# Kernel optimization log

Hardware: AMD Instinct MI355X
Metric: run time of the kernel (lower is better)

The kernel has to match this reference:

```python
import jax, jax.numpy as jnp
import numpy as np

NUM_NODES_G1 = 60000
NUM_NODES_G2 = 50000
NUM_REL = 16
NUM_BASES = 4
DIM = 128  # node_dim == hidden_dim == final_dim
L_COMMON = 100


def _concept_layer(x, edge_index):
    # Gather-based concept propagation: x_i <- x_i + mean_{j in N(i)} x_j
    src, dst = edge_index[0], edge_index[1]
    n = x.shape[0]
    agg = jax.ops.segment_sum(x[src], dst, num_segments=n)
    deg = jax.ops.segment_sum(jnp.ones((src.shape[0],), x.dtype), dst, num_segments=n)
    return x + agg / jnp.clip(deg, 1.0)[:, None]


def _rgcn_layer(x, edge_index, edge_type, basis, comp, root, bias):
    # Basis-decomposed RGCN: out_i = x_i @ root + bias + sum_r (1/|N_i^r|) sum_{j in N_i^r} x_j @ W_r,
    # W_r = sum_b comp[r,b] * basis[b]. Reorder: scatter comp-weighted x[src] per basis, then one GEMM per basis.
    src, dst = edge_index[0], edge_index[1]
    n = x.shape[0]
    e = src.shape[0]
    seg = dst * NUM_REL + edge_type  # per-(node, relation) bucket
    cnt = jax.ops.segment_sum(jnp.ones((e,), x.dtype), seg, num_segments=n * NUM_REL)
    norm = 1.0 / jnp.clip(cnt, 1.0)
    coef = comp[edge_type] * norm[seg][:, None]  # [E, B]
    xsrc = x[src]  # [E, D] -- dominant gather traffic
    out = x @ root + bias
    for b in range(NUM_BASES):  # small fixed loop over bases
        agg_b = jax.ops.segment_sum(xsrc * coef[:, b:b + 1], dst, num_segments=n)
        out = out + agg_b @ basis[b]
    return out


def setup_inputs() -> dict:
    key = jax.random.key(0)
    ks = jax.random.split(key, 16)
    e2, e1 = 800000, 800000
    return {
        "edge_index_g2": jax.random.randint(ks[0], (2, e2), 0, NUM_NODES_G2),
        "edge_type_g2": jax.random.randint(ks[1], (e2,), 0, NUM_REL),
        "edge_index_g1": jax.random.randint(ks[2], (2, e1), 0, NUM_NODES_G1),
        "left_common": jax.random.randint(ks[3], (L_COMMON,), 0, NUM_NODES_G1),
        "all_node_embedding": jax.random.normal(ks[4], (NUM_NODES_G1, DIM), jnp.float32),
        "basis1": jax.random.normal(ks[5], (NUM_BASES, DIM, DIM), jnp.float32) * 0.05,
        "comp1": jax.random.normal(ks[6], (NUM_REL, NUM_BASES), jnp.float32),
        "root1": jax.random.normal(ks[7], (DIM, DIM), jnp.float32) * 0.05,
        "bias1": jnp.zeros((DIM,), jnp.float32),
        "basis2": jax.random.normal(ks[8], (NUM_BASES, DIM, DIM), jnp.float32) * 0.05,
        "comp2": jax.random.normal(ks[9], (NUM_REL, NUM_BASES), jnp.float32),
        "root2": jax.random.normal(ks[10], (DIM, DIM), jnp.float32) * 0.05,
        "bias2": jnp.zeros((DIM,), jnp.float32),
        "weights": jax.random.uniform(ks[11], (DIM, 1), jnp.float32),
    }


def reference(edge_index_g2, edge_type_g2, edge_index_g1, left_common,
              all_node_embedding, basis1, comp1, root1, bias1,
              basis2, comp2, root2, bias2, weights):
    x_g1 = jax.nn.relu(_concept_layer(all_node_embedding, edge_index_g1))
    x = x_g1[:NUM_NODES_G2]
    x = _rgcn_layer(x, edge_index_g2, edge_type_g2, basis1, comp1, root1, bias1)
    x = jax.nn.relu(x)  # relu_use == 1
    x_g2 = _rgcn_layer(x, edge_index_g2, edge_type_g2, basis2, comp2, root2, bias2)
    ty = x_g1[left_common]  # [L, D]
    # mul_def outer elementwise product followed by matmul with weights collapses to one contraction:
    # logits[n,l] = sum_d x_g2[n,d] * ty[l,d] * w[d]
    logits = jnp.einsum('nd,ld,d->nl', x_g2, ty, weights[:, 0])
    return jax.nn.softmax(logits, axis=1)
```

## Files before the change

### kernel.cpp

```cpp
#include <hip/hip_runtime.h>
#include <hip/hip_bf16.h>
#include <math.h>

#define N1 60000
#define N2 50000
#define DIM 128
#define NREL 16
#define NB 4
#define LCOM 100
#define LPAD 112

typedef __attribute__((ext_vector_type(8))) short short8;
typedef __attribute__((ext_vector_type(4))) float f32x4;
typedef __attribute__((ext_vector_type(4))) _Float16 half4;

__device__ __forceinline__ float bf2f(unsigned short u) {
    union { unsigned int i; float f; } c; c.i = ((unsigned int)u) << 16; return c.f;
}
__device__ __forceinline__ unsigned short f2bf(float f) {
    union { float f; unsigned int i; } c; c.f = f;
    unsigned int r = c.i + 0x7FFF + ((c.i >> 16) & 1);
    return (unsigned short)(r >> 16);
}
__device__ __forceinline__ void split8(float4 a, float4 b, short8& h, short8& l) {
    float f[8] = {a.x, a.y, a.z, a.w, b.x, b.y, b.z, b.w};
#pragma unroll
    for (int j = 0; j < 8; j++) {
        unsigned short hh = f2bf(f[j]);
        h[j] = (short)hh;
        l[j] = (short)f2bf(f[j] - bf2f(hh));
    }
}

__global__ void k_cast_emb(const float* __restrict__ emb, _Float16* __restrict__ embh, int n4) {
    int i = blockIdx.x * blockDim.x + threadIdx.x;
    if (i >= n4) return;
    float4 v = ((const float4*)emb)[i];
    half4 o = {(_Float16)v.x, (_Float16)v.y, (_Float16)v.z, (_Float16)v.w};
    ((half4*)embh)[i] = o;
}

__global__ void k_prep_w2(const float* __restrict__ root1, const float* __restrict__ basis1,
                          unsigned short* __restrict__ Wh1, unsigned short* __restrict__ Wl1,
                          const float* __restrict__ root2, const float* __restrict__ basis2,
                          unsigned short* __restrict__ Wh2, unsigned short* __restrict__ Wl2) {
    int t = blockIdx.x * blockDim.x + threadIdx.x;
    if (t >= 2 * 640 * 128) return;
    int which = t >= 640 * 128;
    int tt = which ? t - 640 * 128 : t;
    const float* root = which ? root2 : root1;
    const float* basis = which ? basis2 : basis1;
    unsigned short* Wh = which ? Wh2 : Wh1;
    unsigned short* Wl = which ? Wl2 : Wl1;
    int k = tt >> 7, n = tt & 127;
    float v = (k < 128) ? root[k * 128 + n] : basis[(k - 128) * 128 + n];
    unsigned short h = f2bf(v);
    Wh[n * 640 + k] = h;
    Wl[n * 640 + k] = f2bf(v - bf2f(h));
}

__global__ void k_hist_both(const int* __restrict__ ei1, int E1, int* __restrict__ deg1,
                            const int* __restrict__ ei2, int E2, int* __restrict__ deg2) {
    int g = blockIdx.x * blockDim.x + threadIdx.x;
    if (g < E1) atomicAdd(deg1 + ei1[E1 + g], 1);
    if (g < E2) atomicAdd(deg2 + ei2[E2 + g], 1);
}

__global__ __launch_bounds__(256) void k_scan_p1m(const int* __restrict__ inA, int nA, int nbA,
                                                  int* __restrict__ bsumA,
                                                  const int* __restrict__ inB, int nB,
                                                  int* __restrict__ bsumB) {
    __shared__ int red[256];
    const int* in; int n; int* bsum; int b;
    if ((int)blockIdx.x < nbA) { in = inA; n = nA; bsum = bsumA; b = blockIdx.x; }
    else { in = inB; n = nB; bsum = bsumB; b = blockIdx.x - nbA; }
    int base = b * 1024;
    int tid = threadIdx.x;
    int s = 0;
#pragma unroll
    for (int j = 0; j < 4; j++) {
        int i = base + tid * 4 + j;
        if (i < n) s += in[i];
    }
    red[tid] = s;
    __syncthreads();
    for (int d = 128; d; d >>= 1) {
        if (tid < d) red[tid] += red[tid + d];
        __syncthreads();
    }
    if (tid == 0) bsum[b] = red[0];
}

__global__ __launch_bounds__(64) void k_scan_p2m(const int* __restrict__ bsumA, int* __restrict__ boffA,
                                                 int* __restrict__ offA, int nbA, int nA,
                                                 const int* __restrict__ bsumB, int* __restrict__ boffB,
                                                 int* __restrict__ offB, int nbB, int nB) {
    __shared__ int s[64];
    const int* bsum; int* boff; int* off; int nb; int n;
    if (blockIdx.x == 0) { bsum = bsumA; boff = boffA; off = offA; nb = nbA; n = nA; }
    else { bsum = bsumB; boff = boffB; off = offB; nb = nbB; n = nB; }
    int tid = threadIdx.x;
    int v = (tid < nb) ? bsum[tid] : 0;
    s[tid] = v;
    __syncthreads();
    for (int d = 1; d < 64; d <<= 1) {
        int t = (tid >= d) ? s[tid - d] : 0;
        __syncthreads();
        s[tid] += t;
        __syncthreads();
    }
    if (tid < nb) boff[tid] = s[tid] - v;
    if (tid == 63) off[n] = s[63];
}

__global__ __launch_bounds__(256) void k_scan_p3m(const int* __restrict__ inA, const int* __restrict__ boffA,
                                                  int* __restrict__ offA, int* __restrict__ curA,
                                                  int nA, int nbA,
                                                  const int* __restrict__ inB, const int* __restrict__ boffB,
                                                  int* __restrict__ offB, int* __restrict__ curB, int nB) {
    __shared__ int red[256];
    const int* in; const int* boff; int* off; int* cur; int n; int b;
    if ((int)blockIdx.x < nbA) { in = inA; boff = boffA; off = offA; cur = curA; n = nA; b = blockIdx.x; }
    else { in = inB; boff = boffB; off = offB; cur = curB; n = nB; b = blockIdx.x - nbA; }
    int base = b * 1024;
    int tid = threadIdx.x;
    int v[4];
    int s = 0;
#pragma unroll
    for (int j = 0; j < 4; j++) {
        int i = base + tid * 4 + j;
        v[j] = (i < n) ? in[i] : 0;
        s += v[j];
    }
    red[tid] = s;
    __syncthreads();
    for (int d = 1; d < 256; d <<= 1) {
        int t = (tid >= d) ? red[tid - d] : 0;
        __syncthreads();
        red[tid] += t;
        __syncthreads();
    }
    int run = boff[b] + red[tid] - s;
#pragma unroll
    for (int j = 0; j < 4; j++) {
        int i = base + tid * 4 + j;
        if (i < n) {
            off[i] = run; cur[i] = run;
            run += v[j];
        }
    }
}

__global__ void k_scat_both(const int* __restrict__ ei1, int E1, int* __restrict__ cur1,
                            int* __restrict__ elist1,
                            const int* __restrict__ ei2, const int* __restrict__ et2, int E2,
                            int* __restrict__ cur2, int* __restrict__ elist2) {
    int g = blockIdx.x * blockDim.x + threadIdx.x;
    if (g < E1) {
        int pos = atomicAdd(cur1 + ei1[E1 + g], 1);
        elist1[pos] = ei1[g];
    }
    if (g < E2) {
        int pos = atomicAdd(cur2 + ei2[E2 + g], 1);
        elist2[pos] = (ei2[g] << 4) | et2[g];
    }
}

__global__ void k_nrm_pack(const int* __restrict__ off, const int* __restrict__ elist,
                           int2* __restrict__ epack, int n) {
    int node = blockIdx.x * blockDim.x + threadIdx.x;
    if (node >= n) return;
    int s0 = off[node], s1 = off[node + 1];
    unsigned long long c0 = 0, c1 = 0;
    for (int i = s0; i < s1; i++) {
        int t = elist[i] & 15;
        if (t < 8) c0 += 1ull << (8 * t); else c1 += 1ull << (8 * (t - 8));
    }
    for (int i = s0; i < s1; i++) {
        int p = elist[i];
        int t = p & 15;
        unsigned int c = (t < 8) ? (unsigned int)((c0 >> (8 * t)) & 255)
                                 : (unsigned int)((c1 >> (8 * (t - 8))) & 255);
        float nrm = 1.0f / (float)max(c, 1u);
        int2 e;
        e.x = p;
        e.y = __float_as_int(nrm);
        epack[i] = e;
    }
}

__global__ __launch_bounds__(256) void k_concept_gather(const _Float16* __restrict__ embh,
                                                        const float* __restrict__ emb,
                                                        const int* __restrict__ off,
                                                        const int* __restrict__ elist,
                                                        float* __restrict__ xg1,
                                                        _Float16* __restrict__ xg1h, int n) {
    int node = blockIdx.x * 4 + (threadIdx.x >> 6);
    int lane = threadIdx.x & 63;
    if (node >= n) return;
    int half = lane >> 5, d4 = (lane & 31) * 4;
    int s0 = off[node], s1 = off[node + 1];
    float4 acc = {0.f, 0.f, 0.f, 0.f};
    int i = s0;
    for (; i + 4 <= s1; i += 4) {
        int sa = elist[i + half];
        int sb = elist[i + 2 + half];
        half4 ha = *(const half4*)(embh + (size_t)sa * DIM + d4);
        half4 hb = *(const half4*)(embh + (size_t)sb * DIM + d4);
        acc.x += (float)ha[0] + (float)hb[0];
        acc.y += (float)ha[1] + (float)hb[1];
        acc.z += (float)ha[2] + (float)hb[2];
        acc.w += (float)ha[3] + (float)hb[3];
    }
    for (; i < s1; i += 2) {
        int e = i + half;
        bool ok = e < s1;
        int s = elist[ok ? e : i];
        half4 hv = *(const half4*)(embh + (size_t)s * DIM + d4);
        if (ok) {
            acc.x += (float)hv[0]; acc.y += (float)hv[1];
            acc.z += (float)hv[2]; acc.w += (float)hv[3];
        }
    }
    acc.x += __shfl_xor(acc.x, 32, 64);
    acc.y += __shfl_xor(acc.y, 32, 64);
    acc.z += __shfl_xor(acc.z, 32, 64);
    acc.w += __shfl_xor(acc.w, 32, 64);
    if (half == 0) {
        float inv = 1.0f / (float)max(s1 - s0, 1);
        float4 e = *(const float4*)(emb + (size_t)node * DIM + d4);
        float4 o = {fmaxf(e.x + acc.x * inv, 0.f), fmaxf(e.y + acc.y * inv, 0.f),
                    fmaxf(e.z + acc.z * inv, 0.f), fmaxf(e.w + acc.w * inv, 0.f)};
        *(float4*)(xg1 + (size_t)node * DIM + d4) = o;
        half4 oh = {(_Float16)o.x, (_Float16)o.y, (_Float16)o.z, (_Float16)o.w};
        *(half4*)(xg1h + (size_t)node * DIM + d4) = oh;
    }
}

__global__ __launch_bounds__(64) void k_tyw(const float* __restrict__ emb,
                                            const int* __restrict__ off,
                                            const int* __restrict__ elist,
                                            const int* __restrict__ lc,
                                            const float* __restrict__ w,
                                            unsigned short* __restrict__ tyh,
                                            unsigned short* __restrict__ tyl) {
    int l = blockIdx.x;
    int lane = threadIdx.x;
    int d0 = lane * 2;
    if (l >= LCOM) {
        ushort2 z = {0, 0};
        *(ushort2*)(tyh + (size_t)l * 128 + d0) = z;
        *(ushort2*)(tyl + (size_t)l * 128 + d0) = z;
        return;
    }
    int row = lc[l];
    int s0 = off[row], s1 = off[row + 1];
    float2 acc = {0.f, 0.f};
    for (int i = s0; i < s1; i++) {
        int s = elist[i];
        float2 v = *(const float2*)(emb + (size_t)s * DIM + lane * 2);
        acc.x += v.x; acc.y += v.y;
    }
    float inv = 1.0f / (float)max(s1 - s0, 1);
    float2 e = *(const float2*)(emb + (size_t)row * DIM + lane * 2);
    float v0 = fmaxf(e.x + acc.x * inv, 0.f) * w[d0];
    float v1 = fmaxf(e.y + acc.y * inv, 0.f) * w[d0 + 1];
    unsigned short h0 = f2bf(v0), h1 = f2bf(v1);
    ushort2 hh = {h0, h1};
    ushort2 ll = {f2bf(v0 - bf2f(h0)), f2bf(v1 - bf2f(h1))};
    *(ushort2*)(tyh + (size_t)l * 128 + d0) = hh;
    *(ushort2*)(tyl + (size_t)l * 128 + d0) = ll;
}

__global__ __launch_bounds__(256) void k_rgcn_gather(const _Float16* __restrict__ xh,
                                                     const int* __restrict__ off,
                                                     const int2* __restrict__ epack,
                                                     const float* __restrict__ comp,
                                                     float* __restrict__ agg, int n) {
    __shared__ float scomp[NREL * NB];
    if (threadIdx.x < NREL * NB) scomp[threadIdx.x] = comp[threadIdx.x];
    __syncthreads();
    int node = blockIdx.x * 4 + (threadIdx.x >> 6);
    int lane = threadIdx.x & 63;
    if (node >= n) return;
    int half = lane >> 5, d4 = (lane & 31) * 4;
    int s0 = off[node], s1 = off[node + 1];
    float4 a0 = {0, 0, 0, 0}, a1 = a0, a2 = a0, a3 = a0;
    int i = s0;
#define RG_EDGE(E_IDX, GATE)                                                   \
    {                                                                          \
        int2 pk = epack[E_IDX];                                                \
        int s = pk.x >> 4, t = pk.x & 15;                                      \
        float nr = __int_as_float(pk.y) * (GATE);                              \
        float4 cf = *(const float4*)(scomp + t * 4);                           \
        half4 hv = *(const half4*)(xh + (size_t)s * DIM + d4);                 \
        float4 v = {(float)hv[0], (float)hv[1], (float)hv[2], (float)hv[3]};   \
        float c0 = cf.x * nr, c1 = cf.y * nr, c2 = cf.z * nr, c3 = cf.w * nr;  \
        a0.x = fmaf(c0, v.x, a0.x); a0.y = fmaf(c0, v.y, a0.y);                \
        a0.z = fmaf(c0, v.z, a0.z); a0.w = fmaf(c0, v.w, a0.w);                \
        a1.x = fmaf(c1, v.x, a1.x); a1.y = fmaf(c1, v.y, a1.y);                \
        a1.z = fmaf(c1, v.z, a1.z); a1.w = fmaf(c1, v.w, a1.w);                \
        a2.x = fmaf(c2, v.x, a2.x); a2.y = fmaf(c2, v.y, a2.y);                \
        a2.z = fmaf(c2, v.z, a2.z); a2.w = fmaf(c2, v.w, a2.w);                \
        a3.x = fmaf(c3, v.x, a3.x); a3.y = fmaf(c3, v.y, a3.y);                \
        a3.z = fmaf(c3, v.z, a3.z); a3.w = fmaf(c3, v.w, a3.w);                \
    }
    for (; i + 4 <= s1; i += 4) {
        RG_EDGE(i + half, 1.0f);
        RG_EDGE(i + 2 + half, 1.0f);
    }
    for (; i < s1; i += 2) {
        int e = i + half;
        bool ok = e < s1;
        int ei_ = ok ? e : i;
        RG_EDGE(ei_, ok ? 1.0f : 0.0f);
    }
#undef RG_EDGE
    a0.x += __shfl_xor(a0.x, 32, 64); a0.y += __shfl_xor(a0.y, 32, 64);
    a0.z += __shfl_xor(a0.z, 32, 64); a0.w += __shfl_xor(a0.w, 32, 64);
    a1.x += __shfl_xor(a1.x, 32, 64); a1.y += __shfl_xor(a1.y, 32, 64);
    a1.z += __shfl_xor(a1.z, 32, 64); a1.w += __shfl_xor(a1.w, 32, 64);
    a2.x += __shfl_xor(a2.x, 32, 64); a2.y += __shfl_xor(a2.y, 32, 64);
    a2.z += __shfl_xor(a2.z, 32, 64); a2.w += __shfl_xor(a2.w, 32, 64);
    a3.x += __shfl_xor(a3.x, 32, 64); a3.y += __shfl_xor(a3.y, 32, 64);
    a3.z += __shfl_xor(a3.z, 32, 64); a3.w += __shfl_xor(a3.w, 32, 64);
    if (half == 0) {
        float* o = agg + (size_t)node * (NB * DIM) + d4;
        *(float4*)(o + 0 * DIM) = a0;
        *(float4*)(o + 1 * DIM) = a1;
        *(float4*)(o + 2 * DIM) = a2;
        *(float4*)(o + 3 * DIM) = a3;
    }
}

#define LDSK 40
__global__ __launch_bounds__(256) void k_gemm(const float* __restrict__ x,
                                              const float* __restrict__ agg,
                                              const unsigned short* __restrict__ Wh,
                                              const unsigned short* __restrict__ Wl,
                                              const float* __restrict__ bias,
                                              float* __restrict__ out,
                                              _Float16* __restrict__ out_h, int relu) {
    __shared__ __align__(16) short Ah[128 * LDSK];
    __shared__ __align__(16) short Al[128 * LDSK];
    __shared__ __align__(16) short Bh[128 * LDSK];
    __shared__ __align__(16) short Bl[128 * LDSK];
    int tid = threadIdx.x;
    int lane = tid & 63, wid = tid >> 6;
    int wave_m = wid >> 1, wave_n = wid & 1;
    int l15 = lane & 15, quad = lane >> 4;
    int row0 = blockIdx.x * 128;

    int srow = tid >> 1, skh = (tid & 1) * 16;

    f32x4 acc[4][4] = {};
    for (int k0 = 0; k0 < 640; k0 += 32) {
        {
            int rg = row0 + srow;
            float4 q0 = {0, 0, 0, 0}, q1 = q0, q2 = q0, q3 = q0;
            if (rg < N2) {
                const float* src = (k0 < 128) ? (x + (size_t)rg * 128 + k0 + skh)
                                              : (agg + (size_t)rg * 512 + (k0 - 128) + skh);
                q0 = *(const float4*)(src + 0);
                q1 = *(const float4*)(src + 4);
                q2 = *(const float4*)(src + 8);
                q3 = *(const float4*)(src + 12);
            }
            short8 h0, l0, h1, l1;
            split8(q0, q1, h0, l0);
            split8(q2, q3, h1, l1);
            *(short8*)(&Ah[srow * LDSK + skh]) = h0;
            *(short8*)(&Ah[srow * LDSK + skh + 8]) = h1;
            *(short8*)(&Al[srow * LDSK + skh]) = l0;
            *(short8*)(&Al[srow * LDSK + skh + 8]) = l1;
        }
        {
            const unsigned short* sh = Wh + (size_t)srow * 640 + k0 + skh;
            const unsigned short* sl = Wl + (size_t)srow * 640 + k0 + skh;
            *(short8*)(&Bh[srow * LDSK + skh]) = *(const short8*)(sh);
            *(short8*)(&Bh[srow * LDSK + skh + 8]) = *(const short8*)(sh + 8);
            *(short8*)(&Bl[srow * LDSK + skh]) = *(const short8*)(sl);
            *(short8*)(&Bl[srow * LDSK + skh + 8]) = *(const short8*)(sl + 8);
        }
        __syncthreads();
        short8 ah[4], al[4], bh[4], bl[4];
#pragma unroll
        for (int i = 0; i < 4; i++) {
            int ro = (wave_m * 64 + i * 16 + l15) * LDSK + quad * 8;
            ah[i] = *(const short8*)(&Ah[ro]);
            al[i] = *(const short8*)(&Al[ro]);
        }
#pragma unroll
        for (int j = 0; j < 4; j++) {
            int ro = (wave_n * 64 + j * 16 + l15) * LDSK + quad * 8;
            bh[j] = *(const short8*)(&Bh[ro]);
            bl[j] = *(const short8*)(&Bl[ro]);
        }
#pragma unroll
        for (int i = 0; i < 4; i++)
#pragma unroll
            for (int j = 0; j < 4; j++) {
                acc[i][j] = __builtin_amdgcn_mfma_f32_16x16x32_bf16(al[i], bh[j], acc[i][j], 0, 0, 0);
                acc[i][j] = __builtin_amdgcn_mfma_f32_16x16x32_bf16(ah[i], bl[j], acc[i][j], 0, 0, 0);
                acc[i][j] = __builtin_amdgcn_mfma_f32_16x16x32_bf16(ah[i], bh[j], acc[i][j], 0, 0, 0);
            }
        __syncthreads();
    }
#pragma unroll
    for (int j = 0; j < 4; j++) {
        int gcol = wave_n * 64 + j * 16 + l15;
        float bv = bias[gcol];
#pragma unroll
        for (int i = 0; i < 4; i++) {
            int grow_base = row0 + wave_m * 64 + i * 16 + quad * 4;
#pragma unroll
            for (int r = 0; r < 4; r++) {
                int grow = grow_base + r;
                if (grow >= N2) continue;
                float v = acc[i][j][r] + bv;
                if (relu) v = fmaxf(v, 0.f);
                out[(size_t)grow * 128 + gcol] = v;
                if (out_h) out_h[(size_t)grow * 128 + gcol] = (_Float16)v;
            }
        }
    }
}

__global__ __launch_bounds__(256) void k_logits(const float* __restrict__ h2,
                                                const unsigned short* __restrict__ tyh,
                                                const unsigned short* __restrict__ tyl,
                                                float* __restrict__ out, int M) {
    int wid = threadIdx.x >> 6, lane = threadIdx.x & 63;
    int l15 = lane & 15, quad = lane >> 4;
    int row0w = blockIdx.x * 64 + wid * 16;
    int arow = min(row0w + l15, M - 1);
    f32x4 acc[7] = {};
#pragma unroll
    for (int k0 = 0; k0 < 128; k0 += 32) {
        const float* ap = h2 + (size_t)arow * 128 + k0 + quad * 8;
        float4 q0 = *(const float4*)(ap);
        float4 q1 = *(const float4*)(ap + 4);
        short8 ah, al;
        split8(q0, q1, ah, al);
#pragma unroll
        for (int j = 0; j < 7; j++) {
            size_t bo = (size_t)(j * 16 + l15) * 128 + k0 + quad * 8;
            short8 bh = *(const short8*)(tyh + bo);
            short8 bl = *(const short8*)(tyl + bo);
            acc[j] = __builtin_amdgcn_mfma_f32_16x16x32_bf16(al, bh, acc[j], 0, 0, 0);
            acc[j] = __builtin_amdgcn_mfma_f32_16x16x32_bf16(ah, bl, acc[j], 0, 0, 0);
            acc[j] = __builtin_amdgcn_mfma_f32_16x16x32_bf16(ah, bh, acc[j], 0, 0, 0);
        }
    }
    bool v6 = (l15 < LCOM - 96);
#pragma unroll
    for (int r = 0; r < 4; r++) {
        int grow = row0w + quad * 4 + r;
        float m = -INFINITY;
#pragma unroll
        for (int j = 0; j < 6; j++) m = fmaxf(m, acc[j][r]);
        if (v6) m = fmaxf(m, acc[6][r]);
        m = fmaxf(m, __shfl_xor(m, 8, 64));
        m = fmaxf(m, __shfl_xor(m, 4, 64));
        m = fmaxf(m, __shfl_xor(m, 2, 64));
        m = fmaxf(m, __shfl_xor(m, 1, 64));
        float e[7];
        float s = 0.f;
#pragma unroll
        for (int j = 0; j < 6; j++) { e[j] = __expf(acc[j][r] - m); s += e[j]; }
        e[6] = v6 ? __expf(acc[6][r] - m) : 0.f;
        s += e[6];
        s += __shfl_xor(s, 8, 64);
        s += __shfl_xor(s, 4, 64);
        s += __shfl_xor(s, 2, 64);
        s += __shfl_xor(s, 1, 64);
        float inv = 1.0f / s;
        if (grow < M) {
#pragma unroll
            for (int j = 0; j < 6; j++) out[(size_t)grow * LCOM + j * 16 + l15] = e[j] * inv;
            if (v6) out[(size_t)grow * LCOM + 96 + l15] = e[6] * inv;
        }
    }
}

extern "C" void kernel_launch(void* const* d_in, const int* in_sizes, int n_in,
                              void* d_out, int out_size, void* d_ws, size_t ws_size,
                              hipStream_t stream) {
    const int* ei2 = (const int*)d_in[0];
    const int* et2 = (const int*)d_in[1];
    const int* ei1 = (const int*)d_in[2];
    const int* lc = (const int*)d_in[3];
    const float* emb = (const float*)d_in[4];
    const float* basis1 = (const float*)d_in[5];
    const float* comp1 = (const float*)d_in[6];
    const float* root1 = (const float*)d_in[7];
    const float* bias1 = (const float*)d_in[8];
    const float* basis2 = (const float*)d_in[9];
    const float* comp2 = (const float*)d_in[10];
    const float* root2 = (const float*)d_in[11];
    const float* bias2 = (const float*)d_in[12];
    const float* wts = (const float*)d_in[13];
    float* out = (float*)d_out;
    int E2 = in_sizes[0] / 2, E1 = in_sizes[2] / 2;

    float* ws = (float*)d_ws;
    float* xg1 = ws;
    float* h1 = xg1 + 6400000;
    float* agg = h1 + 6400000;
    _Float16* emb_h = (_Float16*)(agg + 25600000);
    int2* epack = (int2*)(emb_h + 7680000);
    unsigned short* tyh = (unsigned short*)(epack + 800000);
    unsigned short* tyl = tyh + LPAD * 128;
    unsigned short* Wh1 = tyl + LPAD * 128;
    unsigned short* Wl1 = Wh1 + 81920;
    unsigned short* Wh2 = Wl1 + 81920;
    unsigned short* Wl2 = Wh2 + 81920;
    int* ipool = (int*)(Wl2 + 81920);
    int* deg1 = ipool;
    int* deg2 = deg1 + 60000;
    int* off1 = deg2 + 50000;
    int* cur1 = off1 + 60001;
    int* elist1 = cur1 + 60000;
    int* off2 = elist1 + 800000;
    int* cur2 = off2 + 50001;
    int* elist2 = cur2 + 50000;
    int* bsum1 = elist2 + 800000;
    int* boff1 = bsum1 + 64;
    int* bsum2 = boff1 + 64;
    int* boff2 = bsum2 + 64;
    _Float16* xg1_h = (_Float16*)h1;
    _Float16* h1_h = emb_h;
    float* h2 = xg1;

    const int NB1 = (N1 + 1023) / 1024;
    const int NB2 = (N2 + 1023) / 1024;

    k_prep_w2<<<(2 * 640 * 128 + 255) / 256, 256, 0, stream>>>(root1, basis1, Wh1, Wl1,
                                                               root2, basis2, Wh2, Wl2);
    k_cast_emb<<<(N1 * DIM / 4 + 255) / 256, 256, 0, stream>>>(emb, emb_h, N1 * DIM / 4);
    hipMemsetAsync(deg1, 0, (60000 + 50000) * sizeof(int), stream);

    k_hist_both<<<(max(E1, E2) + 255) / 256, 256, 0, stream>>>(ei1, E1, deg1, ei2, E2, deg2);
    k_scan_p1m<<<NB1 + NB2, 256, 0, stream>>>(deg1, N1, NB1, bsum1, deg2, N2, bsum2);
    k_scan_p2m<<<2, 64, 0, stream>>>(bsum1, boff1, off1, NB1, N1, bsum2, boff2, off2, NB2, N2);
    k_scan_p3m<<<NB1 + NB2, 256, 0, stream>>>(deg1, boff1, off1, cur1, N1, NB1,
                                              deg2, boff2, off2, cur2, N2);
    k_scat_both<<<(max(E1, E2) + 255) / 256, 256, 0, stream>>>(ei1, E1, cur1, elist1,
                                                               ei2, et2, E2, cur2, elist2);
    k_nrm_pack<<<(N2 + 255) / 256, 256, 0, stream>>>(off2, elist2, epack, N2);

    k_concept_gather<<<(N2 + 3) / 4, 256, 0, stream>>>(emb_h, emb, off1, elist1, xg1, xg1_h, N2);
    k_tyw<<<LPAD, 64, 0, stream>>>(emb, off1, elist1, lc, wts, tyh, tyl);

    k_rgcn_gather<<<(N2 + 3) / 4, 256, 0, stream>>>(xg1_h, off2, epack, comp1, agg, N2);
    k_gemm<<<(N2 + 127) / 128, 256, 0, stream>>>(xg1, agg, Wh1, Wl1, bias1, h1, h1_h, 1);

    k_rgcn_gather<<<(N2 + 3) / 4, 256, 0, stream>>>(h1_h, off2, epack, comp2, agg, N2);
    k_gemm<<<(N2 + 127) / 128, 256, 0, stream>>>(h1, agg, Wh2, Wl2, bias2, h2, (_Float16*)nullptr, 0);

    k_logits<<<(N2 + 63) / 64, 256, 0, stream>>>(h2, tyh, tyl, out, N2);
}
```

Before: 597.4 us.

## Merge prelude kernels, fuse concept gather with g2 scatter, compute norms inline

Combines the histogram, weight-split and embedding-cast kernels into one block-partitioned launch. It also co-schedules the concept gather, the graph-2 edge scatter and the ty computation in a single mixed launch, and splits the graph-1 scatter into its own kernel. The separate norm-pack pass and its int2 edge array are removed: each wavefront of the RGCN gather now counts relation types per node with a shuffle reduction and reads norms from LDS. This cuts launch count and edge-list traffic, at the cost of recounting norms in both RGCN layers and mixing heterogeneous work within one grid.

```diff
diff --git a/kernel.cpp b/kernel.cpp
--- a/kernel.cpp
+++ b/kernel.cpp
@@ -32,38 +32,52 @@
     }
 }
 
-__global__ void k_cast_emb(const float* __restrict__ emb, _Float16* __restrict__ embh, int n4) {
-    int i = blockIdx.x * blockDim.x + threadIdx.x;
-    if (i >= n4) return;
-    float4 v = ((const float4*)emb)[i];
-    half4 o = {(_Float16)v.x, (_Float16)v.y, (_Float16)v.z, (_Float16)v.w};
-    ((half4*)embh)[i] = o;
-}
-
-__global__ void k_prep_w2(const float* __restrict__ root1, const float* __restrict__ basis1,
-                          unsigned short* __restrict__ Wh1, unsigned short* __restrict__ Wl1,
-                          const float* __restrict__ root2, const float* __restrict__ basis2,
-                          unsigned short* __restrict__ Wh2, unsigned short* __restrict__ Wl2) {
-    int t = blockIdx.x * blockDim.x + threadIdx.x;
-    if (t >= 2 * 640 * 128) return;
-    int which = t >= 640 * 128;
-    int tt = which ? t - 640 * 128 : t;
-    const float* root = which ? root2 : root1;
-    const float* basis = which ? basis2 : basis1;
-    unsigned short* Wh = which ? Wh2 : Wh1;
-    unsigned short* Wl = which ? Wl2 : Wl1;
-    int k = tt >> 7, n = tt & 127;
-    float v = (k < 128) ? root[k * 128 + n] : basis[(k - 128) * 128 + n];
-    unsigned short h = f2bf(v);
-    Wh[n * 640 + k] = h;
-    Wl[n * 640 + k] = f2bf(v - bf2f(h));
-}
-
-__global__ void k_hist_both(const int* __restrict__ ei1, int E1, int* __restrict__ deg1,
-                            const int* __restrict__ ei2, int E2, int* __restrict__ deg2) {
-    int g = blockIdx.x * blockDim.x + threadIdx.x;
-    if (g < E1) atomicAdd(deg1 + ei1[E1 + g], 1);
-    if (g < E2) atomicAdd(deg2 + ei2[E2 + g], 1);
+__global__ __launch_bounds__(256) void k_prelude(
+        const int* __restrict__ ei1, int E1, int* __restrict__ deg1, int HB1,
+        const int* __restrict__ ei2, int E2, int* __restrict__ deg2, int HB2,
+        const float* __restrict__ root1, const float* __restrict__ basis1,
+        unsigned short* __restrict__ Wh1, unsigned short* __restrict__ Wl1,
+        const float* __restrict__ root2, const float* __restrict__ basis2,
+        unsigned short* __restrict__ Wh2, unsigned short* __restrict__ Wl2, int PB,
+        const float* __restrict__ emb, _Float16* __restrict__ embh, int n4) {
+    int b = blockIdx.x;
+    if (b < HB1) {
+        int e0 = b * 1024 + threadIdx.x;
+#pragma unroll
+        for (int j = 0; j < 4; j++) {
+            int e = e0 + j * 256;
+            if (e < E1) atomicAdd(deg1 + ei1[E1 + e], 1);
+        }
+    } else if (b < HB1 + HB2) {
+        int e0 = (b - HB1) * 1024 + threadIdx.x;
+#pragma unroll
+        for (int j = 0; j < 4; j++) {
+            int e = e0 + j * 256;
+            if (e < E2) atomicAdd(deg2 + ei2[E2 + e], 1);
+        }
+    } else if (b < HB1 + HB2 + PB) {
+        int t = (b - HB1 - HB2) * 256 + threadIdx.x;
+        if (t < 2 * 640 * 128) {
+            int which = t >= 640 * 128;
+            int tt = which ? t - 640 * 128 : t;
+            const float* root = which ? root2 : root1;
+            const float* basis = which ? basis2 : basis1;
+            unsigned short* Wh = which ? Wh2 : Wh1;
+            unsigned short* Wl = which ? Wl2 : Wl1;
+            int k = tt >> 7, n = tt & 127;
+            float v = (k < 128) ? root[k * 128 + n] : basis[(k - 128) * 128 + n];
+            unsigned short h = f2bf(v);
+            Wh[n * 640 + k] = h;
+            Wl[n * 640 + k] = f2bf(v - bf2f(h));
+        }
+    } else {
+        int i = (b - HB1 - HB2 - PB) * 256 + threadIdx.x;
+        if (i < n4) {
+            float4 v = ((const float4*)emb)[i];
+            half4 o = {(_Float16)v.x, (_Float16)v.y, (_Float16)v.z, (_Float16)v.w};
+            ((half4*)embh)[i] = o;
+        }
+    }
 }
 
 __global__ __launch_bounds__(256) void k_scan_p1m(const int* __restrict__ inA, int nA, int nbA,
@@ -151,159 +165,159 @@
     }
 }
 
-__global__ void k_scat_both(const int* __restrict__ ei1, int E1, int* __restrict__ cur1,
-                            int* __restrict__ elist1,
-                            const int* __restrict__ ei2, const int* __restrict__ et2, int E2,
-                            int* __restrict__ cur2, int* __restrict__ elist2) {
-    int g = blockIdx.x * blockDim.x + threadIdx.x;
-    if (g < E1) {
-        int pos = atomicAdd(cur1 + ei1[E1 + g], 1);
-        elist1[pos] = ei1[g];
-    }
-    if (g < E2) {
-        int pos = atomicAdd(cur2 + ei2[E2 + g], 1);
-        elist2[pos] = (ei2[g] << 4) | et2[g];
-    }
-}
-
-__global__ void k_nrm_pack(const int* __restrict__ off, const int* __restrict__ elist,
-                           int2* __restrict__ epack, int n) {
-    int node = blockIdx.x * blockDim.x + threadIdx.x;
+__global__ void k_scat1(const int* __restrict__ ei, int E, int* __restrict__ cur,
+                        int* __restrict__ elist) {
+    int e0 = blockIdx.x * 1024 + threadIdx.x;
+#pragma unroll
+    for (int j = 0; j < 4; j++) {
+        int e = e0 + j * 256;
+        if (e < E) {
+            int pos = atomicAdd(cur + ei[E + e], 1);
+            elist[pos] = ei[e];
+        }
+    }
+}
+
+__global__ __launch_bounds__(256) void k_mix(
+        const _Float16* __restrict__ embh, const float* __restrict__ emb,
+        const int* __restrict__ off1, const int* __restrict__ elist1,
+        float* __restrict__ xg1, _Float16* __restrict__ xg1h, int CONC_B,
+        const int* __restrict__ ei2, const int* __restrict__ et2, int E2,
+        int* __restrict__ cur2, int* __restrict__ elist2, int SC2_B,
+        const int* __restrict__ lc, const float* __restrict__ w,
+        unsigned short* __restrict__ tyh, unsigned short* __restrict__ tyl) {
+    int b = blockIdx.x;
+    if (b < CONC_B) {
+        int node = b * 4 + (threadIdx.x >> 6);
+        int lane = threadIdx.x & 63;
+        if (node >= N2) return;
+        int half = lane >> 5, d4 = (lane & 31) * 4;
+        int s0 = off1[node], s1 = off1[node + 1];
+        float4 acc = {0.f, 0.f, 0.f, 0.f};
+        int i = s0;
+        for (; i + 4 <= s1; i += 4) {
+            int sa = elist1[i + half];
+            int sb = elist1[i + 2 + half];
+            half4 ha = *(const half4*)(embh + (size_t)sa * DIM + d4);
+            half4 hb = *(const half4*)(embh + (size_t)sb * DIM + d4);
+            acc.x += (float)ha[0] + (float)hb[0];
+            acc.y += (float)ha[1] + (float)hb[1];
+            acc.z += (float)ha[2] + (float)hb[2];
+            acc.w += (float)ha[3] + (float)hb[3];
+        }
+        for (; i < s1; i += 2) {
+            int e = i + half;
+            bool ok = e < s1;
+            int s = elist1[ok ? e : i];
+            half4 hv = *(const half4*)(embh + (size_t)s * DIM + d4);
+            if (ok) {
+                acc.x += (float)hv[0]; acc.y += (float)hv[1];
+                acc.z += (float)hv[2]; acc.w += (float)hv[3];
+            }
+        }
+        acc.x += __shfl_xor(acc.x, 32, 64);
+        acc.y += __shfl_xor(acc.y, 32, 64);
+        acc.z += __shfl_xor(acc.z, 32, 64);
+        acc.w += __shfl_xor(acc.w, 32, 64);
+        if (half == 0) {
+            float inv = 1.0f / (float)max(s1 - s0, 1);
+            float4 e = *(const float4*)(emb + (size_t)node * DIM + d4);
+            float4 o = {fmaxf(e.x + acc.x * inv, 0.f), fmaxf(e.y + acc.y * inv, 0.f),
+                        fmaxf(e.z + acc.z * inv, 0.f), fmaxf(e.w + acc.w * inv, 0.f)};
+            *(float4*)(xg1 + (size_t)node * DIM + d4) = o;
+            half4 oh = {(_Float16)o.x, (_Float16)o.y, (_Float16)o.z, (_Float16)o.w};
+            *(half4*)(xg1h + (size_t)node * DIM + d4) = oh;
+        }
+    } else if (b < CONC_B + SC2_B) {
+        int e0 = (b - CONC_B) * 1024 + threadIdx.x;
+#pragma unroll
+        for (int j = 0; j < 4; j++) {
+            int e = e0 + j * 256;
+            if (e < E2) {
+                int pos = atomicAdd(cur2 + ei2[E2 + e], 1);
+                elist2[pos] = (ei2[e] << 4) | et2[e];
+            }
+        }
+    } else {
+        if (threadIdx.x >= 64) return;
+        int l = b - CONC_B - SC2_B;
+        int lane = threadIdx.x;
+        int d0 = lane * 2;
+        if (l >= LCOM) {
+            ushort2 z = {0, 0};
+            *(ushort2*)(tyh + (size_t)l * 128 + d0) = z;
+            *(ushort2*)(tyl + (size_t)l * 128 + d0) = z;
+            return;
+        }
+        int row = lc[l];
+        int s0 = off1[row], s1 = off1[row + 1];
+        float2 acc = {0.f, 0.f};
+        for (int i = s0; i < s1; i++) {
+            int s = elist1[i];
+            float2 v = *(const float2*)(emb + (size_t)s * DIM + lane * 2);
+            acc.x += v.x; acc.y += v.y;
+        }
+        float inv = 1.0f / (float)max(s1 - s0, 1);
+        float2 e = *(const float2*)(emb + (size_t)row * DIM + lane * 2);
+        float v0 = fmaxf(e.x + acc.x * inv, 0.f) * w[d0];
+        float v1 = fmaxf(e.y + acc.y * inv, 0.f) * w[d0 + 1];
+        unsigned short h0 = f2bf(v0), h1 = f2bf(v1);
+        ushort2 hh = {h0, h1};
+        ushort2 ll = {f2bf(v0 - bf2f(h0)), f2bf(v1 - bf2f(h1))};
+        *(ushort2*)(tyh + (size_t)l * 128 + d0) = hh;
+        *(ushort2*)(tyl + (size_t)l * 128 + d0) = ll;
+    }
+}
+
+__global__ __launch_bounds__(256) void k_rgcn_gather(const _Float16* __restrict__ xh,
+                                                     const int* __restrict__ off,
+                                                     const int* __restrict__ elist,
+                                                     const float* __restrict__ comp,
+                                                     float* __restrict__ agg, int n) {
+    __shared__ float scomp[NREL * NB];
+    __shared__ float nrmlds[4][NREL];
+    if (threadIdx.x < NREL * NB) scomp[threadIdx.x] = comp[threadIdx.x];
+    __syncthreads();
+    int nb = threadIdx.x >> 6;
+    int node = blockIdx.x * 4 + nb;
+    int lane = threadIdx.x & 63;
     if (node >= n) return;
     int s0 = off[node], s1 = off[node + 1];
     unsigned long long c0 = 0, c1 = 0;
-    for (int i = s0; i < s1; i++) {
+    for (int i = s0 + lane; i < s1; i += 64) {
         int t = elist[i] & 15;
         if (t < 8) c0 += 1ull << (8 * t); else c1 += 1ull << (8 * (t - 8));
     }
-    for (int i = s0; i < s1; i++) {
-        int p = elist[i];
-        int t = p & 15;
-        unsigned int c = (t < 8) ? (unsigned int)((c0 >> (8 * t)) & 255)
-                                 : (unsigned int)((c1 >> (8 * (t - 8))) & 255);
-        float nrm = 1.0f / (float)max(c, 1u);
-        int2 e;
-        e.x = p;
-        e.y = __float_as_int(nrm);
-        epack[i] = e;
-    }
-}
-
-__global__ __launch_bounds__(256) void k_concept_gather(const _Float16* __restrict__ embh,
-                                                        const float* __restrict__ emb,
-                                                        const int* __restrict__ off,
-                                                        const int* __restrict__ elist,
-                                                        float* __restrict__ xg1,
-                                                        _Float16* __restrict__ xg1h, int n) {
-    int node = blockIdx.x * 4 + (threadIdx.x >> 6);
-    int lane = threadIdx.x & 63;
-    if (node >= n) return;
+#pragma unroll
+    for (int o = 32; o; o >>= 1) {
+        c0 += __shfl_xor(c0, o, 64);
+        c1 += __shfl_xor(c1, o, 64);
+    }
+    if (lane < NREL) {
+        unsigned int c = (lane < 8) ? (unsigned int)((c0 >> (8 * lane)) & 255)
+                                    : (unsigned int)((c1 >> (8 * (lane - 8))) & 255);
+        nrmlds[nb][lane] = 1.0f / (float)max(c, 1u);
+    }
     int half = lane >> 5, d4 = (lane & 31) * 4;
-    int s0 = off[node], s1 = off[node + 1];
-    float4 acc = {0.f, 0.f, 0.f, 0.f};
-    int i = s0;
-    for (; i + 4 <= s1; i += 4) {
-        int sa = elist[i + half];
-        int sb = elist[i + 2 + half];
-        half4 ha = *(const half4*)(embh + (size_t)sa * DIM + d4);
-        half4 hb = *(const half4*)(embh + (size_t)sb * DIM + d4);
-        acc.x += (float)ha[0] + (float)hb[0];
-        acc.y += (float)ha[1] + (float)hb[1];
-        acc.z += (float)ha[2] + (float)hb[2];
-        acc.w += (float)ha[3] + (float)hb[3];
-    }
-    for (; i < s1; i += 2) {
-        int e = i + half;
-        bool ok = e < s1;
-        int s = elist[ok ? e : i];
-        half4 hv = *(const half4*)(embh + (size_t)s * DIM + d4);
-        if (ok) {
-            acc.x += (float)hv[0]; acc.y += (float)hv[1];
-            acc.z += (float)hv[2]; acc.w += (float)hv[3];
-        }
-    }
-    acc.x += __shfl_xor(acc.x, 32, 64);
-    acc.y += __shfl_xor(acc.y, 32, 64);
-    acc.z += __shfl_xor(acc.z, 32, 64);
-    acc.w += __shfl_xor(acc.w, 32, 64);
-    if (half == 0) {
-        float inv = 1.0f / (float)max(s1 - s0, 1);
-        float4 e = *(const float4*)(emb + (size_t)node * DIM + d4);
-        float4 o = {fmaxf(e.x + acc.x * inv, 0.f), fmaxf(e.y + acc.y * inv, 0.f),
-                    fmaxf(e.z + acc.z * inv, 0.f), fmaxf(e.w + acc.w * inv, 0.f)};
-        *(float4*)(xg1 + (size_t)node * DIM + d4) = o;
-        half4 oh = {(_Float16)o.x, (_Float16)o.y, (_Float16)o.z, (_Float16)o.w};
-        *(half4*)(xg1h + (size_t)node * DIM + d4) = oh;
-    }
-}
-
-__global__ __launch_bounds__(64) void k_tyw(const float* __restrict__ emb,
-                                            const int* __restrict__ off,
-                                            const int* __restrict__ elist,
-                                            const int* __restrict__ lc,
-                                            const float* __restrict__ w,
-                                            unsigned short* __restrict__ tyh,
-                                            unsigned short* __restrict__ tyl) {
-    int l = blockIdx.x;
-    int lane = threadIdx.x;
-    int d0 = lane * 2;
-    if (l >= LCOM) {
-        ushort2 z = {0, 0};
-        *(ushort2*)(tyh + (size_t)l * 128 + d0) = z;
-        *(ushort2*)(tyl + (size_t)l * 128 + d0) = z;
-        return;
-    }
-    int row = lc[l];
-    int s0 = off[row], s1 = off[row + 1];
-    float2 acc = {0.f, 0.f};
-    for (int i = s0; i < s1; i++) {
-        int s = elist[i];
-        float2 v = *(const float2*)(emb + (size_t)s * DIM + lane * 2);
-        acc.x += v.x; acc.y += v.y;
-    }
-    float inv = 1.0f / (float)max(s1 - s0, 1);
-    float2 e = *(const float2*)(emb + (size_t)row * DIM + lane * 2);
-    float v0 = fmaxf(e.x + acc.x * inv, 0.f) * w[d0];
-    float v1 = fmaxf(e.y + acc.y * inv, 0.f) * w[d0 + 1];
-    unsigned short h0 = f2bf(v0), h1 = f2bf(v1);
-    ushort2 hh = {h0, h1};
-    ushort2 ll = {f2bf(v0 - bf2f(h0)), f2bf(v1 - bf2f(h1))};
-    *(ushort2*)(tyh + (size_t)l * 128 + d0) = hh;
-    *(ushort2*)(tyl + (size_t)l * 128 + d0) = ll;
-}
-
-__global__ __launch_bounds__(256) void k_rgcn_gather(const _Float16* __restrict__ xh,
-                                                     const int* __restrict__ off,
-                                                     const int2* __restrict__ epack,
-                                                     const float* __restrict__ comp,
-                                                     float* __restrict__ agg, int n) {
-    __shared__ float scomp[NREL * NB];
-    if (threadIdx.x < NREL * NB) scomp[threadIdx.x] = comp[threadIdx.x];
-    __syncthreads();
-    int node = blockIdx.x * 4 + (threadIdx.x >> 6);
-    int lane = threadIdx.x & 63;
-    if (node >= n) return;
-    int half = lane >> 5, d4 = (lane & 31) * 4;
-    int s0 = off[node], s1 = off[node + 1];
     float4 a0 = {0, 0, 0, 0}, a1 = a0, a2 = a0, a3 = a0;
     int i = s0;
 #define RG_EDGE(E_IDX, GATE)                                                   \
     {                                                                          \
-        int2 pk = epack[E_IDX];                                                \
-        int s = pk.x >> 4, t = pk.x & 15;                                      \
-        float nr = __int_as_float(pk.y) * (GATE);                              \
+        int p = elist[E_IDX];                                                  \
+        int s = p >> 4, t = p & 15;                                            \
+        float nr = nrmlds[nb][t] * (GATE);                                     \
         float4 cf = *(const float4*)(scomp + t * 4);                           \
         half4 hv = *(const half4*)(xh + (size_t)s * DIM + d4);                 \
         float4 v = {(float)hv[0], (float)hv[1], (float)hv[2], (float)hv[3]};   \
-        float c0 = cf.x * nr, c1 = cf.y * nr, c2 = cf.z * nr, c3 = cf.w * nr;  \
-        a0.x = fmaf(c0, v.x, a0.x); a0.y = fmaf(c0, v.y, a0.y);                \
-        a0.z = fmaf(c0, v.z, a0.z); a0.w = fmaf(c0, v.w, a0.w);                \
-        a1.x = fmaf(c1, v.x, a1.x); a1.y = fmaf(c1, v.y, a1.y);                \
-        a1.z = fmaf(c1, v.z, a1.z); a1.w = fmaf(c1, v.w, a1.w);                \
-        a2.x = fmaf(c2, v.x, a2.x); a2.y = fmaf(c2, v.y, a2.y);                \
-        a2.z = fmaf(c2, v.z, a2.z); a2.w = fmaf(c2, v.w, a2.w);                \
-        a3.x = fmaf(c3, v.x, a3.x); a3.y = fmaf(c3, v.y, a3.y);                \
-        a3.z = fmaf(c3, v.z, a3.z); a3.w = fmaf(c3, v.w, a3.w);                \
+        float c0_ = cf.x * nr, c1_ = cf.y * nr, c2_ = cf.z * nr, c3_ = cf.w * nr; \
+        a0.x = fmaf(c0_, v.x, a0.x); a0.y = fmaf(c0_, v.y, a0.y);              \
+        a0.z = fmaf(c0_, v.z, a0.z); a0.w = fmaf(c0_, v.w, a0.w);              \
+        a1.x = fmaf(c1_, v.x, a1.x); a1.y = fmaf(c1_, v.y, a1.y);              \
+        a1.z = fmaf(c1_, v.z, a1.z); a1.w = fmaf(c1_, v.w, a1.w);              \
+        a2.x = fmaf(c2_, v.x, a2.x); a2.y = fmaf(c2_, v.y, a2.y);              \
+        a2.z = fmaf(c2_, v.z, a2.z); a2.w = fmaf(c2_, v.w, a2.w);              \
+        a3.x = fmaf(c3_, v.x, a3.x); a3.y = fmaf(c3_, v.y, a3.y);              \
+        a3.z = fmaf(c3_, v.z, a3.z); a3.w = fmaf(c3_, v.w, a3.w);              \
     }
     for (; i + 4 <= s1; i += 4) {
         RG_EDGE(i + half, 1.0f);
@@ -508,8 +522,7 @@
     float* h1 = xg1 + 6400000;
     float* agg = h1 + 6400000;
     _Float16* emb_h = (_Float16*)(agg + 25600000);
-    int2* epack = (int2*)(emb_h + 7680000);
-    unsigned short* tyh = (unsigned short*)(epack + 800000);
+    unsigned short* tyh = (unsigned short*)(emb_h + 7680000);
     unsigned short* tyl = tyh + LPAD * 128;
     unsigned short* Wh1 = tyl + LPAD * 128;
     unsigned short* Wl1 = Wh1 + 81920;
@@ -534,28 +547,36 @@
 
     const int NB1 = (N1 + 1023) / 1024;
     const int NB2 = (N2 + 1023) / 1024;
-
-    k_prep_w2<<<(2 * 640 * 128 + 255) / 256, 256, 0, stream>>>(root1, basis1, Wh1, Wl1,
-                                                               root2, basis2, Wh2, Wl2);
-    k_cast_emb<<<(N1 * DIM / 4 + 255) / 256, 256, 0, stream>>>(emb, emb_h, N1 * DIM / 4);
+    const int HB1 = (E1 + 1023) / 1024;
+    const int HB2 = (E2 + 1023) / 1024;
+    const int PB = (2 * 640 * 128) / 256;
+    const int CB = (N1 * DIM / 4 + 255) / 256;
+    const int CONC_B = (N2 + 3) / 4;
+    const int SC2_B = HB2;
+
     hipMemsetAsync(deg1, 0, (60000 + 50000) * sizeof(int), stream);
 
-    k_hist_both<<<(max(E1, E2) + 255) / 256, 256, 0, stream>>>(ei1, E1, deg1, ei2, E2, deg2);
+    k_prelude<<<HB1 + HB2 + PB + CB, 256, 0, stream>>>(
+        ei1, E1, deg1, HB1, ei2, E2, deg2, HB2,
+        root1, basis1, Wh1, Wl1, root2, basis2, Wh2, Wl2, PB,
+        emb, emb_h, N1 * DIM / 4);
+
     k_scan_p1m<<<NB1 + NB2, 256, 0, stream>>>(deg1, N1, NB1, bsum1, deg2, N2, bsum2);
     k_scan_p2m<<<2, 64, 0, stream>>>(bsum1, boff1, off1, NB1, N1, bsum2, boff2, off2, NB2, N2);
     k_scan_p3m<<<NB1 + NB2, 256, 0, stream>>>(deg1, boff1, off1, cur1, N1, NB1,
                                               deg2, boff2, off2, cur2, N2);
-    k_scat_both<<<(max(E1, E2) + 255) / 256, 256, 0, stream>>>(ei1, E1, cur1, elist1,
-                                                               ei2, et2, E2, cur2, elist2);
-    k_nrm_pack<<<(N2 + 255) / 256, 256, 0, stream>>>(off2, elist2, epack, N2);
-
-    k_concept_gather<<<(N2 + 3) / 4, 256, 0, stream>>>(emb_h, emb, off1, elist1, xg1, xg1_h, N2);
-    k_tyw<<<LPAD, 64, 0, stream>>>(emb, off1, elist1, lc, wts, tyh, tyl);
-
-    k_rgcn_gather<<<(N2 + 3) / 4, 256, 0, stream>>>(xg1_h, off2, epack, comp1, agg, N2);
+
+    k_scat1<<<HB1, 256, 0, stream>>>(ei1, E1, cur1, elist1);
+
+    k_mix<<<CONC_B + SC2_B + LPAD, 256, 0, stream>>>(
+        emb_h, emb, off1, elist1, xg1, xg1_h, CONC_B,
+        ei2, et2, E2, cur2, elist2, SC2_B,
+        lc, wts, tyh, tyl);
+
+    k_rgcn_gather<<<CONC_B, 256, 0, stream>>>(xg1_h, off2, elist2, comp1, agg, N2);
     k_gemm<<<(N2 + 127) / 128, 256, 0, stream>>>(xg1, agg, Wh1, Wl1, bias1, h1, h1_h, 1);
 
-    k_rgcn_gather<<<(N2 + 3) / 4, 256, 0, stream>>>(h1_h, off2, epack, comp2, agg, N2);
+    k_rgcn_gather<<<CONC_B, 256, 0, stream>>>(h1_h, off2, elist2, comp2, agg, N2);
     k_gemm<<<(N2 + 127) / 128, 256, 0, stream>>>(h1, agg, Wh2, Wl2, bias2, h2, (_Float16*)nullptr, 0);
 
     k_logits<<<(N2 + 63) / 64, 256, 0, stream>>>(h2, tyh, tyl, out, N2);
```

New measurement: 563.5 us. 5.7% less time.
